# Performance work log

Hardware: AMD Instinct MI355X
Metric: run time of the kernel (lower is better)

The kernel has to match this reference:

```python
import jax, jax.numpy as jnp
import numpy as np

IN_SIZE = 4096   # input_size
OUT_SIZE = 4096  # output_size
RANK = 1024      # len(S_4), multiple of 32
GROUPSIZE = 128
BITS = 4
PACK = 32 // BITS  # 8 nibbles per int32
MAXQ_MASK = (1 << BITS) - 1  # 15


def _dequant4(qweight, qzeros, scales, g_idx):
    """GPTQ 4-bit dequant. qweight: int32 [K//8, N]; qzeros: int32 [G, N//8];
    scales: [G, N]; g_idx: int32 [K]. Returns W [K, N] with
    W[k, n] = (int4[k, n] - (zero4[g_idx[k], n] + 1)) * scales[g_idx[k], n]."""
    shifts = (jnp.arange(PACK, dtype=jnp.int32) * BITS)
    K = qweight.shape[0] * PACK
    N = qweight.shape[1]
    # unpack along rows: [K//8, 8, N] -> [K, N]
    intw = ((qweight[:, None, :] >> shifts[None, :, None]) & MAXQ_MASK).reshape(K, N)
    # unpack along cols: [G, N//8, 8] -> [G, N]; pack() stored zeros-1, so add 1 back
    zeros = ((qzeros[:, :, None] >> shifts[None, None, :]) & MAXQ_MASK).reshape(qzeros.shape[0], N) + 1
    sc = scales[g_idx]            # [K, N]
    zr = zeros[g_idx].astype(scales.dtype)  # [K, N]
    return (intw.astype(scales.dtype) - zr) * sc


def setup_inputs() -> dict:
    key = jax.random.key(0)
    ks = jax.random.split(key, 9)
    qweight_V = jax.random.randint(ks[0], (IN_SIZE // PACK, RANK), 0, 2**31 - 1, dtype=jnp.int32)
    qzeros_V = jax.random.randint(ks[1], (IN_SIZE // GROUPSIZE, RANK // PACK), 0, 2**31 - 1, dtype=jnp.int32)
    scales_V = jax.random.uniform(ks[2], (IN_SIZE // GROUPSIZE, RANK), dtype=jnp.float32) * 0.01 + 1e-3
    g_idx_V = (jnp.arange(IN_SIZE, dtype=jnp.int32) // GROUPSIZE).astype(jnp.int32)
    qweight_U = jax.random.randint(ks[3], (RANK // PACK, OUT_SIZE), 0, 2**31 - 1, dtype=jnp.int32)
    qzeros_U = jax.random.randint(ks[4], (RANK // GROUPSIZE, OUT_SIZE // PACK), 0, 2**31 - 1, dtype=jnp.int32)
    scales_U = jax.random.uniform(ks[5], (RANK // GROUPSIZE, OUT_SIZE), dtype=jnp.float32) * 0.01 + 1e-3
    g_idx_U = (jnp.arange(RANK, dtype=jnp.int32) // GROUPSIZE).astype(jnp.int32)
    S = jax.random.uniform(ks[6], (RANK,), dtype=jnp.float32) + 0.1  # singular values
    x = jax.random.normal(ks[7], (4, 2048, IN_SIZE), dtype=jnp.float32)
    return {"x": x,
            "qweight_V": qweight_V, "qzeros_V": qzeros_V, "scales_V": scales_V, "g_idx_V": g_idx_V,
            "qweight_U": qweight_U, "qzeros_U": qzeros_U, "scales_U": scales_U, "g_idx_U": g_idx_U,
            "S": S}


def reference(x, qweight_V, qzeros_V, scales_V, g_idx_V,
              qweight_U, qzeros_U, scales_U, g_idx_U, S):
    # weight_V: dequantized [IN_SIZE, RANK]; weight_U: dequantized [RANK, OUT_SIZE]
    weight_V = _dequant4(qweight_V, qzeros_V, scales_V, g_idx_V)
    weight_U = _dequant4(qweight_U, qzeros_U, scales_U, g_idx_U)
    # forward returns (weight_V @ diag(S) @ weight_U).T  -> [OUT_SIZE, IN_SIZE]
    # (the x @ W_V @ diag(S) @ W_U activation path in the source is dead code
    #  w.r.t. the returned value)
    return ((weight_V * S[None, :]) @ weight_U).T
```

## Files before the change

kernel.cpp:

```cpp
#include <hip/hip_runtime.h>

typedef __attribute__((ext_vector_type(8))) short bf16x8;
typedef __attribute__((ext_vector_type(4))) float f32x4;

__device__ __forceinline__ short f2bf(float f) {
  unsigned u = __builtin_bit_cast(unsigned, f);
  u += 0x7fffu + ((u >> 16) & 1u);
  return (short)(u >> 16);
}


__global__ __launch_bounds__(256) void dequant_v(const int* __restrict__ qw,
                                                 const int* __restrict__ qz,
                                                 const float* __restrict__ sc,
                                                 const float* __restrict__ S,
                                                 short* __restrict__ A) {
  const int t    = blockIdx.x * 256 + threadIdx.x;
  const int tile = t >> 11;
  const int blk  = (t >> 6) & 31;
  const int lane = t & 63;
  const int panel = tile >> 4, kt = tile & 15;
  const int m  = (panel << 8) + (((blk >> 4) & 1) << 7) + (((blk >> 1) & 7) << 4) + (lane & 15);
  const int r0 = (kt << 6) + ((blk & 1) << 5) + ((lane >> 4) << 3);

  const int g  = m >> 7;
  const int sh = (m & 7) << 2;
  const int zw = qz[(g << 7) + (r0 >> 3)];
  const int*   wq  = qw + (m >> 3) * 1024 + r0;
  const float* scp = sc + (g << 10) + r0;
  const float* sp  = S + r0;
  bf16x8 res;
#pragma unroll
  for (int e = 0; e < 8; ++e) {
    int q = (wq[e] >> sh) & 15;
    int z = ((zw >> (e << 2)) & 15) + 1;
    res[e] = f2bf((float)(q - z) * scp[e] * sp[e]);
  }
  *(bf16x8*)(A + ((size_t)t << 3)) = res;
}

__global__ __launch_bounds__(256) void dequant_u(const int* __restrict__ qw,
                                                 const int* __restrict__ qz,
                                                 const float* __restrict__ sc,
                                                 short* __restrict__ B) {
  const int t    = blockIdx.x * 256 + threadIdx.x;
  const int tile = t >> 11;
  const int blk  = (t >> 6) & 31;
  const int lane = t & 63;
  const int panel = tile >> 4, kt = tile & 15;
  const int n  = (panel << 8) + (((blk >> 3) & 3) << 6) + (((blk >> 1) & 3) << 4) + (lane & 15);
  const int r0 = (kt << 6) + ((blk & 1) << 5) + ((lane >> 4) << 3);

  const int w  = qw[(r0 >> 3) * 4096 + n];
  const int g  = r0 >> 7;
  const int zw = qz[(g << 9) + (n >> 3)];
  const int z  = ((zw >> ((n & 7) << 2)) & 15) + 1;
  const float s = sc[(g << 12) + n];
  bf16x8 res;
#pragma unroll
  for (int e = 0; e < 8; ++e) {
    int q = (w >> (e << 2)) & 15;
    res[e] = f2bf((float)(q - z) * s);
  }
  *(bf16x8*)(B + ((size_t)t << 3)) = res;
}

#define GLL(g, l)                                                              \
  __builtin_amdgcn_global_load_lds(                                            \
      (const __attribute__((address_space(1))) void*)(g),                      \
      (__attribute__((address_space(3))) void*)(l), 16, 0, 0)

__global__ __launch_bounds__(512, 2) void gemm256(const short* __restrict__ A,
                                                  const short* __restrict__ B,
                                                  float* __restrict__ out) {
  __shared__ __align__(16) char lds[131072];
  const int tid  = threadIdx.x;
  const int lane = tid & 63;
  const int wid  = tid >> 6;
  const int wm   = wid >> 2;
  const int wn   = wid & 3;
  const int mp = blockIdx.x >> 4;
  const int np = blockIdx.x & 15;

  const short* gA = A + ((size_t)(mp * 16) << 14) + (wid << 11) + (lane << 3);
  const short* gB = B + ((size_t)(np * 16) << 14) + (wid << 11) + (lane << 3);

#define STGA(buf, ktv) do {                                                    \
    const short* s_ = gA + ((ktv) << 14);                                      \
    char* d_ = lds + (buf) + (wid << 12);                                      \
    GLL(s_,        d_);                                                        \
    GLL(s_ +  512, d_ + 1024);                                                 \
    GLL(s_ + 1024, d_ + 2048);                                                 \
    GLL(s_ + 1536, d_ + 3072);                                                 \
  } while (0)
#define STGB(buf, ktv) do {                                                    \
    const short* s_ = gB + ((ktv) << 14);                                      \
    char* d_ = lds + (buf) + 32768 + (wid << 12);                              \
    GLL(s_,        d_);                                                        \
    GLL(s_ +  512, d_ + 1024);                                                 \
    GLL(s_ + 1024, d_ + 2048);                                                 \
    GLL(s_ + 1536, d_ + 3072);                                                 \
  } while (0)

  const char* Ard = lds + (wm << 14) + (lane << 4);
  const char* Brd = lds + 32768 + (wn << 13) + (lane << 4);

  f32x4 acc[8][4];
#pragma unroll
  for (int mi = 0; mi < 8; ++mi)
#pragma unroll
    for (int ni = 0; ni < 4; ++ni) acc[mi][ni] = f32x4{0.f, 0.f, 0.f, 0.f};

  bf16x8 ah[4][2], bh0[2][2], bh1[2][2];

  STGB(0, 0);
  STGA(0, 0);
  STGB(65536, 1);
  STGA(65536, 1);
  asm volatile("s_waitcnt vmcnt(8)" ::: "memory");
  __builtin_amdgcn_s_barrier();

  for (int kt = 0; kt < 16; ++kt) {
    const int curbuf = (kt & 1) << 16;

#pragma unroll
    for (int i = 0; i < 4; ++i) {
      ah[i][0] = *(const bf16x8*)(Ard + curbuf + (i << 11));
      ah[i][1] = *(const bf16x8*)(Ard + curbuf + (i << 11) + 1024);
    }
#pragma unroll
    for (int j = 0; j < 2; ++j) {
      bh0[j][0] = *(const bf16x8*)(Brd + curbuf + (j << 11));
      bh0[j][1] = *(const bf16x8*)(Brd + curbuf + (j << 11) + 1024);
    }
    asm volatile("s_waitcnt lgkmcnt(0)" ::: "memory");
    __builtin_amdgcn_sched_barrier(0);
    __builtin_amdgcn_s_setprio(1);
#pragma unroll
    for (int kk = 0; kk < 2; ++kk)
#pragma unroll
      for (int i = 0; i < 4; ++i)
#pragma unroll
        for (int j = 0; j < 2; ++j)
          acc[i][j] = __builtin_amdgcn_mfma_f32_16x16x32_bf16(
              ah[i][kk], bh0[j][kk], acc[i][j], 0, 0, 0);
    __builtin_amdgcn_s_setprio(0);
    __builtin_amdgcn_s_barrier();

#pragma unroll
    for (int j = 0; j < 2; ++j) {
      bh1[j][0] = *(const bf16x8*)(Brd + curbuf + 4096 + (j << 11));
      bh1[j][1] = *(const bf16x8*)(Brd + curbuf + 4096 + (j << 11) + 1024);
    }
    asm volatile("s_waitcnt lgkmcnt(0)" ::: "memory");
    __builtin_amdgcn_sched_barrier(0);
    __builtin_amdgcn_s_setprio(1);
#pragma unroll
    for (int kk = 0; kk < 2; ++kk)
#pragma unroll
      for (int i = 0; i < 4; ++i)
#pragma unroll
        for (int j = 0; j < 2; ++j)
          acc[i][2 + j] = __builtin_amdgcn_mfma_f32_16x16x32_bf16(
              ah[i][kk], bh1[j][kk], acc[i][2 + j], 0, 0, 0);
    __builtin_amdgcn_s_setprio(0);
    __builtin_amdgcn_s_barrier();

#pragma unroll
    for (int i = 0; i < 4; ++i) {
      ah[i][0] = *(const bf16x8*)(Ard + curbuf + 8192 + (i << 11));
      ah[i][1] = *(const bf16x8*)(Ard + curbuf + 8192 + (i << 11) + 1024);
    }
    if (kt < 14) STGB(curbuf, kt + 2);
    asm volatile("s_waitcnt lgkmcnt(0)" ::: "memory");
    __builtin_amdgcn_sched_barrier(0);
    __builtin_amdgcn_s_setprio(1);
#pragma unroll
    for (int kk = 0; kk < 2; ++kk)
#pragma unroll
      for (int i = 0; i < 4; ++i)
#pragma unroll
        for (int j = 0; j < 2; ++j)
          acc[4 + i][2 + j] = __builtin_amdgcn_mfma_f32_16x16x32_bf16(
              ah[i][kk], bh1[j][kk], acc[4 + i][2 + j], 0, 0, 0);
    __builtin_amdgcn_s_setprio(0);
    __builtin_amdgcn_s_barrier();

    if (kt < 14) STGA(curbuf, kt + 2);
    __builtin_amdgcn_s_setprio(1);
#pragma unroll
    for (int kk = 0; kk < 2; ++kk)
#pragma unroll
      for (int i = 0; i < 4; ++i)
#pragma unroll
        for (int j = 0; j < 2; ++j)
          acc[4 + i][j] = __builtin_amdgcn_mfma_f32_16x16x32_bf16(
              ah[i][kk], bh0[j][kk], acc[4 + i][j], 0, 0, 0);
    __builtin_amdgcn_s_setprio(0);
    if (kt == 14) asm volatile("s_waitcnt vmcnt(0)" ::: "memory");
    else          asm volatile("s_waitcnt vmcnt(8)" ::: "memory");
    __builtin_amdgcn_s_barrier();
  }

  const int mbase = (mp << 8) + (wm << 7) + ((lane >> 4) << 2);
  const int nbase = (np << 8) + (wn << 6) + (lane & 15);
#pragma unroll
  for (int mi = 0; mi < 8; ++mi)
#pragma unroll
    for (int ni = 0; ni < 4; ++ni)
      *(f32x4*)(out + (size_t)(nbase + ni * 16) * 4096 + mbase + mi * 16) =
          acc[mi][ni];
#undef STGA
#undef STGB
}

extern "C" void kernel_launch(void* const* d_in, const int* in_sizes, int n_in,
                              void* d_out, int out_size, void* d_ws, size_t ws_size,
                              hipStream_t stream) {
  const int*   qw_V = (const int*)d_in[1];
  const int*   qz_V = (const int*)d_in[2];
  const float* sc_V = (const float*)d_in[3];
  const int*   qw_U = (const int*)d_in[5];
  const int*   qz_U = (const int*)d_in[6];
  const float* sc_U = (const float*)d_in[7];
  const float* S    = (const float*)d_in[9];

  short* A = (short*)d_ws;
  short* B = (short*)d_ws + 4096 * 1024;
  float* out = (float*)d_out;

  dequant_v<<<2048, 256, 0, stream>>>(qw_V, qz_V, sc_V, S, A);
  dequant_u<<<2048, 256, 0, stream>>>(qw_U, qz_U, sc_U, B);
  gemm256<<<256, 512, 0, stream>>>(A, B, out);
}
```

Before: 51.44 us.

## Fuse dequant kernels, remap GEMM blocks, and overlap LDS reads with MFMA

Merges the two dequantization kernels into one launch that branches on block index, which removes one kernel launch and the serialization gap between them. Remaps GEMM block indices with an XCD-style swizzle so neighbouring tiles land on the same chiplet for better L2 reuse. Restructures the inner loop to split A fragments into lo/hi registers, issuing the hi A loads while earlier MFMAs run and using partial lgkmcnt waits instead of full drains. It also drops one barrier. The extra fragment registers raise register pressure and could affect occupancy.

```diff
diff --git a/kernel.cpp b/kernel.cpp
--- a/kernel.cpp
+++ b/kernel.cpp
@@ -10,59 +10,56 @@
 }
 
 
-__global__ __launch_bounds__(256) void dequant_v(const int* __restrict__ qw,
-                                                 const int* __restrict__ qz,
-                                                 const float* __restrict__ sc,
-                                                 const float* __restrict__ S,
-                                                 short* __restrict__ A) {
-  const int t    = blockIdx.x * 256 + threadIdx.x;
-  const int tile = t >> 11;
-  const int blk  = (t >> 6) & 31;
-  const int lane = t & 63;
-  const int panel = tile >> 4, kt = tile & 15;
-  const int m  = (panel << 8) + (((blk >> 4) & 1) << 7) + (((blk >> 1) & 7) << 4) + (lane & 15);
-  const int r0 = (kt << 6) + ((blk & 1) << 5) + ((lane >> 4) << 3);
-
-  const int g  = m >> 7;
-  const int sh = (m & 7) << 2;
-  const int zw = qz[(g << 7) + (r0 >> 3)];
-  const int*   wq  = qw + (m >> 3) * 1024 + r0;
-  const float* scp = sc + (g << 10) + r0;
-  const float* sp  = S + r0;
-  bf16x8 res;
-#pragma unroll
-  for (int e = 0; e < 8; ++e) {
-    int q = (wq[e] >> sh) & 15;
-    int z = ((zw >> (e << 2)) & 15) + 1;
-    res[e] = f2bf((float)(q - z) * scp[e] * sp[e]);
+__global__ __launch_bounds__(256) void dequant_fused(
+    const int* __restrict__ qw_V, const int* __restrict__ qz_V,
+    const float* __restrict__ sc_V, const float* __restrict__ S,
+    short* __restrict__ A,
+    const int* __restrict__ qw_U, const int* __restrict__ qz_U,
+    const float* __restrict__ sc_U, short* __restrict__ B) {
+  const int bid = blockIdx.x;
+  if (bid < 2048) {
+    const int t    = bid * 256 + threadIdx.x;
+    const int tile = t >> 11;
+    const int blk  = (t >> 6) & 31;
+    const int lane = t & 63;
+    const int panel = tile >> 4, kt = tile & 15;
+    const int m  = (panel << 8) + (((blk >> 4) & 1) << 7) + (((blk >> 1) & 7) << 4) + (lane & 15);
+    const int r0 = (kt << 6) + ((blk & 1) << 5) + ((lane >> 4) << 3);
+    const int g  = m >> 7;
+    const int sh = (m & 7) << 2;
+    const int zw = qz_V[(g << 7) + (r0 >> 3)];
+    const int*   wq  = qw_V + (m >> 3) * 1024 + r0;
+    const float* scp = sc_V + (g << 10) + r0;
+    const float* sp  = S + r0;
+    bf16x8 res;
+#pragma unroll
+    for (int e = 0; e < 8; ++e) {
+      int q = (wq[e] >> sh) & 15;
+      int z = ((zw >> (e << 2)) & 15) + 1;
+      res[e] = f2bf((float)(q - z) * scp[e] * sp[e]);
+    }
+    *(bf16x8*)(A + ((size_t)t << 3)) = res;
+  } else {
+    const int t    = (bid - 2048) * 256 + threadIdx.x;
+    const int tile = t >> 11;
+    const int blk  = (t >> 6) & 31;
+    const int lane = t & 63;
+    const int panel = tile >> 4, kt = tile & 15;
+    const int n  = (panel << 8) + (((blk >> 3) & 3) << 6) + (((blk >> 1) & 3) << 4) + (lane & 15);
+    const int r0 = (kt << 6) + ((blk & 1) << 5) + ((lane >> 4) << 3);
+    const int w  = qw_U[(r0 >> 3) * 4096 + n];
+    const int g  = r0 >> 7;
+    const int zw = qz_U[(g << 9) + (n >> 3)];
+    const int z  = ((zw >> ((n & 7) << 2)) & 15) + 1;
+    const float s = sc_U[(g << 12) + n];
+    bf16x8 res;
+#pragma unroll
+    for (int e = 0; e < 8; ++e) {
+      int q = (w >> (e << 2)) & 15;
+      res[e] = f2bf((float)(q - z) * s);
+    }
+    *(bf16x8*)(B + ((size_t)t << 3)) = res;
   }
-  *(bf16x8*)(A + ((size_t)t << 3)) = res;
-}
-
-__global__ __launch_bounds__(256) void dequant_u(const int* __restrict__ qw,
-                                                 const int* __restrict__ qz,
-                                                 const float* __restrict__ sc,
-                                                 short* __restrict__ B) {
-  const int t    = blockIdx.x * 256 + threadIdx.x;
-  const int tile = t >> 11;
-  const int blk  = (t >> 6) & 31;
-  const int lane = t & 63;
-  const int panel = tile >> 4, kt = tile & 15;
-  const int n  = (panel << 8) + (((blk >> 3) & 3) << 6) + (((blk >> 1) & 3) << 4) + (lane & 15);
-  const int r0 = (kt << 6) + ((blk & 1) << 5) + ((lane >> 4) << 3);
-
-  const int w  = qw[(r0 >> 3) * 4096 + n];
-  const int g  = r0 >> 7;
-  const int zw = qz[(g << 9) + (n >> 3)];
-  const int z  = ((zw >> ((n & 7) << 2)) & 15) + 1;
-  const float s = sc[(g << 12) + n];
-  bf16x8 res;
-#pragma unroll
-  for (int e = 0; e < 8; ++e) {
-    int q = (w >> (e << 2)) & 15;
-    res[e] = f2bf((float)(q - z) * s);
-  }
-  *(bf16x8*)(B + ((size_t)t << 3)) = res;
 }
 
 #define GLL(g, l)                                                              \
@@ -79,8 +76,9 @@
   const int wid  = tid >> 6;
   const int wm   = wid >> 2;
   const int wn   = wid & 3;
-  const int mp = blockIdx.x >> 4;
-  const int np = blockIdx.x & 15;
+  const int bid = ((blockIdx.x & 7) << 5) | (blockIdx.x >> 3);
+  const int mp = bid >> 4;
+  const int np = bid & 15;
 
   const short* gA = A + ((size_t)(mp * 16) << 14) + (wid << 11) + (lane << 3);
   const short* gB = B + ((size_t)(np * 16) << 14) + (wid << 11) + (lane << 3);
@@ -111,7 +109,7 @@
 #pragma unroll
     for (int ni = 0; ni < 4; ++ni) acc[mi][ni] = f32x4{0.f, 0.f, 0.f, 0.f};
 
-  bf16x8 ah[4][2], bh0[2][2], bh1[2][2];
+  bf16x8 alo[4][2], ahi[4][2], bh0[2][2], bh1[2][2];
 
   STGB(0, 0);
   STGA(0, 0);
@@ -125,34 +123,20 @@
 
 #pragma unroll
     for (int i = 0; i < 4; ++i) {
-      ah[i][0] = *(const bf16x8*)(Ard + curbuf + (i << 11));
-      ah[i][1] = *(const bf16x8*)(Ard + curbuf + (i << 11) + 1024);
+      alo[i][0] = *(const bf16x8*)(Ard + curbuf + (i << 11));
+      alo[i][1] = *(const bf16x8*)(Ard + curbuf + (i << 11) + 1024);
     }
 #pragma unroll
     for (int j = 0; j < 2; ++j) {
       bh0[j][0] = *(const bf16x8*)(Brd + curbuf + (j << 11));
       bh0[j][1] = *(const bf16x8*)(Brd + curbuf + (j << 11) + 1024);
     }
-    asm volatile("s_waitcnt lgkmcnt(0)" ::: "memory");
-    __builtin_amdgcn_sched_barrier(0);
-    __builtin_amdgcn_s_setprio(1);
-#pragma unroll
-    for (int kk = 0; kk < 2; ++kk)
-#pragma unroll
-      for (int i = 0; i < 4; ++i)
-#pragma unroll
-        for (int j = 0; j < 2; ++j)
-          acc[i][j] = __builtin_amdgcn_mfma_f32_16x16x32_bf16(
-              ah[i][kk], bh0[j][kk], acc[i][j], 0, 0, 0);
-    __builtin_amdgcn_s_setprio(0);
-    __builtin_amdgcn_s_barrier();
-
 #pragma unroll
     for (int j = 0; j < 2; ++j) {
       bh1[j][0] = *(const bf16x8*)(Brd + curbuf + 4096 + (j << 11));
       bh1[j][1] = *(const bf16x8*)(Brd + curbuf + 4096 + (j << 11) + 1024);
     }
-    asm volatile("s_waitcnt lgkmcnt(0)" ::: "memory");
+    asm volatile("s_waitcnt lgkmcnt(4)" ::: "memory");
     __builtin_amdgcn_sched_barrier(0);
     __builtin_amdgcn_s_setprio(1);
 #pragma unroll
@@ -161,16 +145,29 @@
       for (int i = 0; i < 4; ++i)
 #pragma unroll
         for (int j = 0; j < 2; ++j)
+          acc[i][j] = __builtin_amdgcn_mfma_f32_16x16x32_bf16(
+              alo[i][kk], bh0[j][kk], acc[i][j], 0, 0, 0);
+    __builtin_amdgcn_s_setprio(0);
+
+#pragma unroll
+    for (int i = 0; i < 4; ++i) {
+      ahi[i][0] = *(const bf16x8*)(Ard + curbuf + 8192 + (i << 11));
+      ahi[i][1] = *(const bf16x8*)(Ard + curbuf + 8192 + (i << 11) + 1024);
+    }
+    asm volatile("s_waitcnt lgkmcnt(8)" ::: "memory");
+    __builtin_amdgcn_sched_barrier(0);
+    __builtin_amdgcn_s_setprio(1);
+#pragma unroll
+    for (int kk = 0; kk < 2; ++kk)
+#pragma unroll
+      for (int i = 0; i < 4; ++i)
+#pragma unroll
+        for (int j = 0; j < 2; ++j)
           acc[i][2 + j] = __builtin_amdgcn_mfma_f32_16x16x32_bf16(
-              ah[i][kk], bh1[j][kk], acc[i][2 + j], 0, 0, 0);
+              alo[i][kk], bh1[j][kk], acc[i][2 + j], 0, 0, 0);
     __builtin_amdgcn_s_setprio(0);
     __builtin_amdgcn_s_barrier();
 
-#pragma unroll
-    for (int i = 0; i < 4; ++i) {
-      ah[i][0] = *(const bf16x8*)(Ard + curbuf + 8192 + (i << 11));
-      ah[i][1] = *(const bf16x8*)(Ard + curbuf + 8192 + (i << 11) + 1024);
-    }
     if (kt < 14) STGB(curbuf, kt + 2);
     asm volatile("s_waitcnt lgkmcnt(0)" ::: "memory");
     __builtin_amdgcn_sched_barrier(0);
@@ -182,7 +179,7 @@
 #pragma unroll
         for (int j = 0; j < 2; ++j)
           acc[4 + i][2 + j] = __builtin_amdgcn_mfma_f32_16x16x32_bf16(
-              ah[i][kk], bh1[j][kk], acc[4 + i][2 + j], 0, 0, 0);
+              ahi[i][kk], bh1[j][kk], acc[4 + i][2 + j], 0, 0, 0);
     __builtin_amdgcn_s_setprio(0);
     __builtin_amdgcn_s_barrier();
 
@@ -195,7 +192,7 @@
 #pragma unroll
         for (int j = 0; j < 2; ++j)
           acc[4 + i][j] = __builtin_amdgcn_mfma_f32_16x16x32_bf16(
-              ah[i][kk], bh0[j][kk], acc[4 + i][j], 0, 0, 0);
+              ahi[i][kk], bh0[j][kk], acc[4 + i][j], 0, 0, 0);
     __builtin_amdgcn_s_setprio(0);
     if (kt == 14) asm volatile("s_waitcnt vmcnt(0)" ::: "memory");
     else          asm volatile("s_waitcnt vmcnt(8)" ::: "memory");
@@ -229,7 +226,7 @@
   short* B = (short*)d_ws + 4096 * 1024;
   float* out = (float*)d_out;
 
-  dequant_v<<<2048, 256, 0, stream>>>(qw_V, qz_V, sc_V, S, A);
-  dequant_u<<<2048, 256, 0, stream>>>(qw_U, qz_U, sc_U, B);
+  dequant_fused<<<4096, 256, 0, stream>>>(qw_V, qz_V, sc_V, S, A,
+                                          qw_U, qz_U, sc_U, B);
   gemm256<<<256, 512, 0, stream>>>(A, B, out);
 }
```

Measured after the change: 51.68 us. Within noise of the previous version (+0.5%).
